# Optimization experiments

Measured on AMD Instinct MI355X. Metric: run time of the kernel, lower is better.

## Reference

```python
import jax, jax.numpy as jnp
import numpy as np

INPUT_SIZE = 128
HIDDEN_SIZE = 1024
OUTPUT_SIZE = 64
E_PROP = 0.8
E_SIZE = int(E_PROP * HIDDEN_SIZE)  # 819
I_SIZE = HIDDEN_SIZE - E_SIZE       # 205


def _make_mask():
    # rows of [+1]*E_SIZE + [-1]*I_SIZE, zero diagonal (no self-connection)
    row = np.concatenate([np.ones(E_SIZE), -np.ones(I_SIZE)]).astype(np.float32)
    mask = np.tile(row, (HIDDEN_SIZE, 1))
    np.fill_diagonal(mask, 0.0)
    return jnp.asarray(mask)


def setup_inputs() -> dict:
    key = jax.random.key(0)
    ks = jax.random.split(key, 8)
    T, B = 512, 64
    scale = 1.0 / np.sqrt(HIDDEN_SIZE)
    x = jax.random.normal(ks[0], (T, B, INPUT_SIZE), dtype=jnp.float32)
    w_ih = jax.random.normal(ks[1], (HIDDEN_SIZE, INPUT_SIZE), dtype=jnp.float32) / np.sqrt(INPUT_SIZE)
    b_ih = jax.random.uniform(ks[2], (HIDDEN_SIZE,), minval=-scale, maxval=scale, dtype=jnp.float32)
    w_hh = jax.random.normal(ks[3], (HIDDEN_SIZE, HIDDEN_SIZE), dtype=jnp.float32) * scale
    # mimic reset_parameters: shrink excitatory columns by e_size/i_size ratio
    w_hh = w_hh.at[:, :E_SIZE].divide(E_SIZE / I_SIZE)
    b_hh = jax.random.uniform(ks[4], (HIDDEN_SIZE,), minval=-scale, maxval=scale, dtype=jnp.float32)
    w_fc = jax.random.normal(ks[5], (OUTPUT_SIZE, E_SIZE), dtype=jnp.float32) / np.sqrt(E_SIZE)
    b_fc = jax.random.uniform(ks[6], (OUTPUT_SIZE,), minval=-scale, maxval=scale, dtype=jnp.float32)
    # NOTE: RNN.__init__ hard-codes alpha = 1 regardless of the value passed in.
    alpha = jnp.array([1.0], dtype=jnp.float32)
    mask = _make_mask()
    return {"x": x, "w_ih": w_ih, "b_ih": b_ih, "w_hh": w_hh, "b_hh": b_hh,
            "w_fc": w_fc, "b_fc": b_fc, "alpha": alpha, "mask": mask}


def reference(x, w_ih, b_ih, w_hh, b_hh, w_fc, b_fc, alpha, mask):
    # x: (T, B, I). Precompute input projection for all timesteps (one big GEMM).
    inp_proj = jnp.einsum('tbi,hi->tbh', x, w_ih) + b_ih  # (T, B, H)
    # effective E-I weight: sign-constrained, zero diagonal; constant across steps
    eff_w = jnp.abs(w_hh) * mask                           # (H, H)
    a = alpha[0]
    B = x.shape[1]
    state0 = jnp.zeros((B, HIDDEN_SIZE), dtype=x.dtype)
    out0 = jnp.zeros((B, HIDDEN_SIZE), dtype=x.dtype)

    def step(carry, u_t):
        state, output = carry
        total = u_t + output @ eff_w.T + b_hh             # (B, H)
        state = a * (total - state) + state               # alpha blend (sigma_rec = 0)
        output = jnp.tanh(state)
        return (state, output), output

    _, rnn_activity = jax.lax.scan(step, (state0, out0), inp_proj)  # (T, B, H)
    rnn_e = rnn_activity[:, :, :E_SIZE]                   # excitatory readout only
    out = jnp.einsum('tbe,oe->tbo', rnn_e, w_fc) + b_fc   # (T, B, O)
    return out, rnn_activity
```

## Files before the change

### kernel.cpp

```cpp
#include <hip/hip_runtime.h>
#include <cmath>

#define T_STEPS 512
#define BATCH   64
#define HID     1024
#define INSZ    128
#define ESZ     819
#define OSZ     64

#define WS_EFFW   0
#define WS_WIHT   1048576
#define WS_HIST   1179648
#define WS_FLAGS  34734080
#define WS_WFCP   34742272

__global__ void prep_effw(const float* __restrict__ w_hh, const float* __restrict__ mask,
                          float* __restrict__ eff) {
    const int i = (blockIdx.x * 256 + threadIdx.x) * 4;
    const float4 w = *(const float4*)(w_hh + i);
    const float4 m = *(const float4*)(mask + i);
    float4 r;
    r.x = fabsf(w.x) * m.x; r.y = fabsf(w.y) * m.y;
    r.z = fabsf(w.z) * m.z; r.w = fabsf(w.w) * m.w;
    *(float4*)(eff + i) = r;
}

__global__ void prep_wihT(const float* __restrict__ w_ih, float* __restrict__ w_ihT) {
    const int idx = blockIdx.x * 256 + threadIdx.x;
    const int i = idx >> 10, h = idx & 1023;
    w_ihT[idx] = w_ih[h * INSZ + i];
}

__global__ void prep_wfc(const float* __restrict__ w_fc, float* __restrict__ w_fcp) {
    const int o = blockIdx.x;
    for (int e = threadIdx.x; e < 820; e += 256)
        w_fcp[o * 820 + e] = (e < ESZ) ? w_fc[o * ESZ + e] : 0.f;
}

__global__ void inp_proj(const float* __restrict__ x, const float* __restrict__ w_ihT,
                         const float* __restrict__ b_ih, float* __restrict__ u) {
    __shared__ float xs[INSZ * 64];
    const int t = blockIdx.x, tid = threadIdx.x;
    const float* xt = x + (size_t)t * BATCH * INSZ;
    for (int k = tid * 4; k < BATCH * INSZ; k += 1024) {
        const float4 v = *(const float4*)(xt + k);
        const int b = k >> 7, i = k & 127;
        xs[(i + 0) * 64 + b] = v.x; xs[(i + 1) * 64 + b] = v.y;
        xs[(i + 2) * 64 + b] = v.z; xs[(i + 3) * 64 + b] = v.w;
    }
    __syncthreads();
    for (int hp = 0; hp < 2; ++hp) {
        const int h = hp * 512 + tid * 2;
        const float bi0 = b_ih[h], bi1 = b_ih[h + 1];
        for (int b0 = 0; b0 < 64; b0 += 8) {
            float acc0[8], acc1[8];
#pragma unroll
            for (int bb = 0; bb < 8; ++bb) { acc0[bb] = 0.f; acc1[bb] = 0.f; }
#pragma unroll 4
            for (int i = 0; i < INSZ; ++i) {
                const float2 w2 = *(const float2*)(w_ihT + i * 1024 + h);
                const float4 xa = *(const float4*)(xs + i * 64 + b0);
                const float4 xb = *(const float4*)(xs + i * 64 + b0 + 4);
                const float xv[8] = {xa.x, xa.y, xa.z, xa.w, xb.x, xb.y, xb.z, xb.w};
#pragma unroll
                for (int bb = 0; bb < 8; ++bb) {
                    acc0[bb] = fmaf(w2.x, xv[bb], acc0[bb]);
                    acc1[bb] = fmaf(w2.y, xv[bb], acc1[bb]);
                }
            }
#pragma unroll
            for (int bb = 0; bb < 8; ++bb) {
                float2 r; r.x = acc0[bb] + bi0; r.y = acc1[bb] + bi1;
                *(float2*)(u + ((size_t)(b0 + bb) * T_STEPS + t) * 1024 + h) = r;
            }
        }
    }
}

__global__ void __launch_bounds__(256, 1)
rnn_scan(const float* __restrict__ eff_w, const float* __restrict__ u,
         const float* __restrict__ b_hh, const float* __restrict__ alpha,
         float* __restrict__ hist, unsigned* __restrict__ flags) {
    extern __shared__ float smem[];
    float* w_s = smem;
    float* pp  = smem + 32768;
    const int tid = threadIdx.x, wg = blockIdx.x;
    const int bg = wg & 7, hgrp = wg >> 3;
    const int h0 = hgrp << 5, b0 = bg << 3;

    {
        const int hl = tid >> 3, grp = hl >> 2, l4 = hl & 3;
        const int j0 = (tid & 7) << 7;
        const float* wrow = eff_w + (size_t)(h0 + hl) * 1024;
        for (int j = j0; j < j0 + 128; j += 4) {
            const float4 w4 = *(const float4*)(wrow + j);
            w_s[((j + 0) << 5) + (((grp + j + 0) & 7) << 2) + l4] = w4.x;
            w_s[((j + 1) << 5) + (((grp + j + 1) & 7) << 2) + l4] = w4.y;
            w_s[((j + 2) << 5) + (((grp + j + 2) & 7) << 2) + l4] = w4.z;
            w_s[((j + 3) << 5) + (((grp + j + 3) & 7) << 2) + l4] = w4.w;
        }
    }
    const float a = alpha[0];
    const int r_hl = tid >> 3, r_b = tid & 7;
    const int rh = h0 + r_hl, rb = b0 + r_b;
    const float bias = b_hh[rh];
    const size_t u_base = ((size_t)rb * T_STEPS) * 1024 + rh;
    float* const my_hist = hist + ((size_t)rb * T_STEPS) * 1024 + rh;
    const int hp = tid >> 5, jc = tid & 31;
    const int sb = tid >> 5, sj = (tid & 31) << 5;
    float state = 0.f;
    __syncthreads();

    for (int t = 0; t < T_STEPS; ++t) {
        const float uval = u[u_base + ((size_t)t << 10)];
        float red = 0.f;
        if (t > 0) {
            {
                const float* src = hist + ((size_t)(b0 + sb) * T_STEPS + (t - 1)) * 1024 + sj;
                float* dst = pp + (sb << 10) + sj;
#pragma unroll
                for (int k = 0; k < 32; k += 4)
                    *(float4*)(dst + k) = *(const float4*)(src + k);
            }
            __syncthreads();
            float acc[4][8];
#pragma unroll
            for (int i = 0; i < 4; ++i)
#pragma unroll
                for (int b = 0; b < 8; ++b) acc[i][b] = 0.f;
#pragma unroll 2
            for (int jj = 0; jj < 32; ++jj) {
                const int j = (jj << 5) + jc;
                const float4 wv = *(const float4*)&w_s[(j << 5) + (((hp + j) & 7) << 2)];
                float pv[8];
#pragma unroll
                for (int b = 0; b < 8; ++b) pv[b] = pp[(b << 10) + j];
#pragma unroll
                for (int b = 0; b < 8; ++b) {
                    acc[0][b] = fmaf(wv.x, pv[b], acc[0][b]);
                    acc[1][b] = fmaf(wv.y, pv[b], acc[1][b]);
                    acc[2][b] = fmaf(wv.z, pv[b], acc[2][b]);
                    acc[3][b] = fmaf(wv.w, pv[b], acc[3][b]);
                }
            }
            __syncthreads();
#pragma unroll
            for (int i = 0; i < 4; ++i)
#pragma unroll
                for (int b = 0; b < 8; ++b) {
                    const int oo = ((hp << 2) + i) * 8 + b;
                    pp[(oo << 5) + ((jc + oo) & 31)] = acc[i][b];
                }
            __syncthreads();
#pragma unroll
            for (int k = 0; k < 32; ++k)
                red += pp[(tid << 5) + ((k + tid) & 31)];
        }
        const float tot = uval + bias + red;
        state = fmaf(a, tot - state, state);
        const float ov = tanhf(state);
        __hip_atomic_store(my_hist + ((size_t)t << 10), ov, __ATOMIC_RELAXED,
                           __HIP_MEMORY_SCOPE_AGENT);
        asm volatile("s_waitcnt vmcnt(0)" ::: "memory");
        __syncthreads();
        if (tid == 0)
            __hip_atomic_store(flags + (wg << 5), (unsigned)(t + 1), __ATOMIC_RELAXED,
                               __HIP_MEMORY_SCOPE_AGENT);
        if (tid < 64) {
            const unsigned tgt = (unsigned)(t + 1);
            for (;;) {
                unsigned v = tgt;
                if (tid < 32)
                    v = __hip_atomic_load(flags + ((bg + (tid << 3)) << 5), __ATOMIC_RELAXED,
                                          __HIP_MEMORY_SCOPE_AGENT);
                if (__ballot(v >= tgt) == ~0ull) break;
                __builtin_amdgcn_s_sleep(4);
            }
        }
        __syncthreads();
    }
}

__global__ void copy_act(const float* __restrict__ hist, float* __restrict__ act) {
    const int t = blockIdx.x >> 6, b = blockIdx.x & 63;
    const float* src = hist + ((size_t)b * T_STEPS + t) * 1024 + threadIdx.x * 4;
    float* dst = act + ((size_t)t * BATCH + b) * 1024 + threadIdx.x * 4;
    *(float4*)dst = *(const float4*)src;
}

__global__ void fc_out(const float* __restrict__ hist, const float* __restrict__ w_fcp,
                       const float* __restrict__ b_fc, float* __restrict__ out0) {
    __shared__ float hs[16 * 820];
    const int t = blockIdx.x >> 2, bq = blockIdx.x & 3, tid = threadIdx.x;
    const int b0 = bq << 4;
    for (int r = 0; r < 16; ++r) {
        const float* src = hist + ((size_t)(b0 + r) * T_STEPS + t) * 1024;
        for (int e = tid; e < 820; e += 256) hs[r * 820 + e] = (e < ESZ) ? src[e] : 0.f;
    }
    __syncthreads();
    const int bb = tid >> 4, ol = tid & 15;
    float acc[4] = {0.f, 0.f, 0.f, 0.f};
    const float* hrow = hs + bb * 820;
    for (int e = 0; e < 820; e += 4) {
        const float4 hv = *(const float4*)(hrow + e);
#pragma unroll
        for (int k = 0; k < 4; ++k) {
            const float4 wv = *(const float4*)(w_fcp + (size_t)(ol + (k << 4)) * 820 + e);
            acc[k] += hv.x * wv.x + hv.y * wv.y + hv.z * wv.z + hv.w * wv.w;
        }
    }
    const int b = b0 + bb;
#pragma unroll
    for (int k = 0; k < 4; ++k) {
        const int o = ol + (k << 4);
        out0[((size_t)t * BATCH + b) * OSZ + o] = acc[k] + b_fc[o];
    }
}

extern "C" void kernel_launch(void* const* d_in, const int* in_sizes, int n_in,
                              void* d_out, int out_size, void* d_ws, size_t ws_size,
                              hipStream_t stream) {
    const float* x     = (const float*)d_in[0];
    const float* w_ih  = (const float*)d_in[1];
    const float* b_ih  = (const float*)d_in[2];
    const float* w_hh  = (const float*)d_in[3];
    const float* b_hh  = (const float*)d_in[4];
    const float* w_fc  = (const float*)d_in[5];
    const float* b_fc  = (const float*)d_in[6];
    const float* alpha = (const float*)d_in[7];
    const float* mask  = (const float*)d_in[8];

    float* out  = (float*)d_out;
    float* out0 = out;
    float* act  = out + (size_t)T_STEPS * BATCH * OSZ;

    float* ws     = (float*)d_ws;
    float* eff_w  = ws + WS_EFFW;
    float* w_ihT  = ws + WS_WIHT;
    float* hist   = ws + WS_HIST;
    unsigned* flags = (unsigned*)(ws + WS_FLAGS);
    float* w_fcp  = ws + WS_WFCP;
    float* u      = act;

    hipMemsetAsync(flags, 0, 8192 * sizeof(unsigned), stream);
    prep_effw<<<1024, 256, 0, stream>>>(w_hh, mask, eff_w);
    prep_wihT<<<512, 256, 0, stream>>>(w_ih, w_ihT);
    prep_wfc<<<64, 256, 0, stream>>>(w_fc, w_fcp);
    inp_proj<<<512, 256, 0, stream>>>(x, w_ihT, b_ih, u);

    hipFuncSetAttribute(reinterpret_cast<const void*>(rnn_scan),
                        hipFuncAttributeMaxDynamicSharedMemorySize, 163840);
    void* args[] = {(void*)&eff_w, (void*)&u, (void*)&b_hh, (void*)&alpha,
                    (void*)&hist, (void*)&flags};
    hipLaunchCooperativeKernel(reinterpret_cast<const void*>(rnn_scan),
                               dim3(256), dim3(256), args, 163840, stream);

    copy_act<<<32768, 256, 0, stream>>>(hist, act);
    fc_out<<<2048, 256, 0, stream>>>(hist, w_fcp, b_fc, out0);
}
```

Baseline: 4.452 ms.

## Replace flag barrier with data-embedded readiness via offset-encoded hidden outputs

Removes the per-step flag-based grid barrier. Each output is stored with a +2 offset, so any value of at least 1 marks it as ready, and consumers spin on the data itself. The offset is folded back out algebraically through adjusted biases in the recurrence (row sums of eff_w) and in the readout (row sums of w_fc), and subtracted in copy_act. This needs a full memset of the history buffer and adds rounding error from the offset, and it also adds an LDS swizzle for the pp staging buffer.

```diff
diff --git a/kernel.cpp b/kernel.cpp
--- a/kernel.cpp
+++ b/kernel.cpp
@@ -11,8 +11,10 @@
 #define WS_EFFW   0
 #define WS_WIHT   1048576
 #define WS_HIST   1179648
-#define WS_FLAGS  34734080
+#define WS_BADJ   34734080
 #define WS_WFCP   34742272
+
+typedef float f32x4 __attribute__((ext_vector_type(4)));
 
 __global__ void prep_effw(const float* __restrict__ w_hh, const float* __restrict__ mask,
                           float* __restrict__ eff) {
@@ -31,10 +33,23 @@
     w_ihT[idx] = w_ih[h * INSZ + i];
 }
 
-__global__ void prep_wfc(const float* __restrict__ w_fc, float* __restrict__ w_fcp) {
-    const int o = blockIdx.x;
-    for (int e = threadIdx.x; e < 820; e += 256)
-        w_fcp[o * 820 + e] = (e < ESZ) ? w_fc[o * ESZ + e] : 0.f;
+__global__ void prep_wfc(const float* __restrict__ w_fc, const float* __restrict__ b_fc,
+                         float* __restrict__ w_fcp, float* __restrict__ badj) {
+    __shared__ float red[256];
+    const int o = blockIdx.x, tid = threadIdx.x;
+    float s = 0.f;
+    for (int e = tid; e < 820; e += 256) {
+        const float w = (e < ESZ) ? w_fc[o * ESZ + e] : 0.f;
+        w_fcp[o * 820 + e] = w;
+        s += w;
+    }
+    red[tid] = s;
+    __syncthreads();
+    for (int st = 128; st; st >>= 1) {
+        if (tid < st) red[tid] += red[tid + st];
+        __syncthreads();
+    }
+    if (tid == 0) badj[o] = b_fc[o] - 2.0f * red[0];
 }
 
 __global__ void inp_proj(const float* __restrict__ x, const float* __restrict__ w_ihT,
@@ -77,10 +92,32 @@
     }
 }
 
+#define LOAD8(SFX)                                                       \
+    asm volatile("global_load_dwordx4 %0, %8, off" SFX "\n\t"            \
+                 "global_load_dwordx4 %1, %8, off offset:16" SFX "\n\t"  \
+                 "global_load_dwordx4 %2, %8, off offset:32" SFX "\n\t"  \
+                 "global_load_dwordx4 %3, %8, off offset:48" SFX "\n\t"  \
+                 "global_load_dwordx4 %4, %8, off offset:64" SFX "\n\t"  \
+                 "global_load_dwordx4 %5, %8, off offset:80" SFX "\n\t"  \
+                 "global_load_dwordx4 %6, %8, off offset:96" SFX "\n\t"  \
+                 "global_load_dwordx4 %7, %8, off offset:112" SFX "\n\t" \
+                 "s_waitcnt vmcnt(0)"                                    \
+                 : "=&v"(v0), "=&v"(v1), "=&v"(v2), "=&v"(v3),           \
+                   "=&v"(v4), "=&v"(v5), "=&v"(v6), "=&v"(v7)            \
+                 : "v"(src) : "memory")
+
+__device__ __forceinline__ float vmin4f(f32x4 v) {
+    return fminf(fminf(v[0], v[1]), fminf(v[2], v[3]));
+}
+
+#define MIN32()                                                              \
+    fminf(fminf(fminf(vmin4f(v0), vmin4f(v1)), fminf(vmin4f(v2), vmin4f(v3))), \
+          fminf(fminf(vmin4f(v4), vmin4f(v5)), fminf(vmin4f(v6), vmin4f(v7))))
+
 __global__ void __launch_bounds__(256, 1)
 rnn_scan(const float* __restrict__ eff_w, const float* __restrict__ u,
          const float* __restrict__ b_hh, const float* __restrict__ alpha,
-         float* __restrict__ hist, unsigned* __restrict__ flags) {
+         float* __restrict__ hist) {
     extern __shared__ float smem[];
     float* w_s = smem;
     float* pp  = smem + 32768;
@@ -88,6 +125,7 @@
     const int bg = wg & 7, hgrp = wg >> 3;
     const int h0 = hgrp << 5, b0 = bg << 3;
 
+    float rsum = 0.f;
     {
         const int hl = tid >> 3, grp = hl >> 2, l4 = hl & 3;
         const int j0 = (tid & 7) << 7;
@@ -98,16 +136,24 @@
             w_s[((j + 1) << 5) + (((grp + j + 1) & 7) << 2) + l4] = w4.y;
             w_s[((j + 2) << 5) + (((grp + j + 2) & 7) << 2) + l4] = w4.z;
             w_s[((j + 3) << 5) + (((grp + j + 3) & 7) << 2) + l4] = w4.w;
+            rsum += (w4.x + w4.y) + (w4.z + w4.w);
         }
     }
+    rsum += __shfl_xor(rsum, 1);
+    rsum += __shfl_xor(rsum, 2);
+    rsum += __shfl_xor(rsum, 4);
+
     const float a = alpha[0];
     const int r_hl = tid >> 3, r_b = tid & 7;
     const int rh = h0 + r_hl, rb = b0 + r_b;
-    const float bias = b_hh[rh];
+    const float bias0 = b_hh[rh];
+    const float bias_eff = bias0 - 2.0f * rsum;
     const size_t u_base = ((size_t)rb * T_STEPS) * 1024 + rh;
     float* const my_hist = hist + ((size_t)rb * T_STEPS) * 1024 + rh;
     const int hp = tid >> 5, jc = tid & 31;
     const int sb = tid >> 5, sj = (tid & 31) << 5;
+    const float* const src_base = hist + ((size_t)(b0 + sb) * T_STEPS) * 1024 + sj;
+    const int rot = tid & 7;
     float state = 0.f;
     __syncthreads();
 
@@ -115,14 +161,26 @@
         const float uval = u[u_base + ((size_t)t << 10)];
         float red = 0.f;
         if (t > 0) {
-            {
-                const float* src = hist + ((size_t)(b0 + sb) * T_STEPS + (t - 1)) * 1024 + sj;
-                float* dst = pp + (sb << 10) + sj;
-#pragma unroll
-                for (int k = 0; k < 32; k += 4)
-                    *(float4*)(dst + k) = *(const float4*)(src + k);
+            f32x4 v0, v1, v2, v3, v4, v5, v6, v7;
+            const float* src = src_base + ((size_t)(t - 1) << 10);
+            LOAD8(" sc0");
+            float mn = MIN32();
+            while (!(mn >= 1.0f)) {
+                __builtin_amdgcn_s_sleep(1);
+                LOAD8(" sc0 sc1");
+                mn = MIN32();
             }
+            float* dst = pp + (sb << 10) + sj;
+            *(f32x4*)(dst + (((rot + 0) & 7) << 2)) = v0;
+            *(f32x4*)(dst + (((rot + 1) & 7) << 2)) = v1;
+            *(f32x4*)(dst + (((rot + 2) & 7) << 2)) = v2;
+            *(f32x4*)(dst + (((rot + 3) & 7) << 2)) = v3;
+            *(f32x4*)(dst + (((rot + 4) & 7) << 2)) = v4;
+            *(f32x4*)(dst + (((rot + 5) & 7) << 2)) = v5;
+            *(f32x4*)(dst + (((rot + 6) & 7) << 2)) = v6;
+            *(f32x4*)(dst + (((rot + 7) & 7) << 2)) = v7;
             __syncthreads();
+
             float acc[4][8];
 #pragma unroll
             for (int i = 0; i < 4; ++i)
@@ -131,16 +189,17 @@
 #pragma unroll 2
             for (int jj = 0; jj < 32; ++jj) {
                 const int j = (jj << 5) + jc;
-                const float4 wv = *(const float4*)&w_s[(j << 5) + (((hp + j) & 7) << 2)];
+                const f32x4 wv = *(const f32x4*)&w_s[(j << 5) + (((hp + j) & 7) << 2)];
+                const int phij = (jj << 5) + ((((jj * 9) + (jc >> 2)) & 7) << 2) + (jc & 3);
                 float pv[8];
 #pragma unroll
-                for (int b = 0; b < 8; ++b) pv[b] = pp[(b << 10) + j];
+                for (int b = 0; b < 8; ++b) pv[b] = pp[(b << 10) + phij];
 #pragma unroll
                 for (int b = 0; b < 8; ++b) {
-                    acc[0][b] = fmaf(wv.x, pv[b], acc[0][b]);
-                    acc[1][b] = fmaf(wv.y, pv[b], acc[1][b]);
-                    acc[2][b] = fmaf(wv.z, pv[b], acc[2][b]);
-                    acc[3][b] = fmaf(wv.w, pv[b], acc[3][b]);
+                    acc[0][b] = fmaf(wv[0], pv[b], acc[0][b]);
+                    acc[1][b] = fmaf(wv[1], pv[b], acc[1][b]);
+                    acc[2][b] = fmaf(wv[2], pv[b], acc[2][b]);
+                    acc[3][b] = fmaf(wv[3], pv[b], acc[3][b]);
                 }
             }
             __syncthreads();
@@ -156,27 +215,11 @@
             for (int k = 0; k < 32; ++k)
                 red += pp[(tid << 5) + ((k + tid) & 31)];
         }
-        const float tot = uval + bias + red;
+        const float tot = uval + red + ((t > 0) ? bias_eff : bias0);
         state = fmaf(a, tot - state, state);
         const float ov = tanhf(state);
-        __hip_atomic_store(my_hist + ((size_t)t << 10), ov, __ATOMIC_RELAXED,
+        __hip_atomic_store(my_hist + ((size_t)t << 10), ov + 2.0f, __ATOMIC_RELAXED,
                            __HIP_MEMORY_SCOPE_AGENT);
-        asm volatile("s_waitcnt vmcnt(0)" ::: "memory");
-        __syncthreads();
-        if (tid == 0)
-            __hip_atomic_store(flags + (wg << 5), (unsigned)(t + 1), __ATOMIC_RELAXED,
-                               __HIP_MEMORY_SCOPE_AGENT);
-        if (tid < 64) {
-            const unsigned tgt = (unsigned)(t + 1);
-            for (;;) {
-                unsigned v = tgt;
-                if (tid < 32)
-                    v = __hip_atomic_load(flags + ((bg + (tid << 3)) << 5), __ATOMIC_RELAXED,
-                                          __HIP_MEMORY_SCOPE_AGENT);
-                if (__ballot(v >= tgt) == ~0ull) break;
-                __builtin_amdgcn_s_sleep(4);
-            }
-        }
         __syncthreads();
     }
 }
@@ -185,11 +228,13 @@
     const int t = blockIdx.x >> 6, b = blockIdx.x & 63;
     const float* src = hist + ((size_t)b * T_STEPS + t) * 1024 + threadIdx.x * 4;
     float* dst = act + ((size_t)t * BATCH + b) * 1024 + threadIdx.x * 4;
-    *(float4*)dst = *(const float4*)src;
+    float4 v = *(const float4*)src;
+    v.x -= 2.0f; v.y -= 2.0f; v.z -= 2.0f; v.w -= 2.0f;
+    *(float4*)dst = v;
 }
 
 __global__ void fc_out(const float* __restrict__ hist, const float* __restrict__ w_fcp,
-                       const float* __restrict__ b_fc, float* __restrict__ out0) {
+                       const float* __restrict__ badj, float* __restrict__ out0) {
     __shared__ float hs[16 * 820];
     const int t = blockIdx.x >> 2, bq = blockIdx.x & 3, tid = threadIdx.x;
     const int b0 = bq << 4;
@@ -213,7 +258,7 @@
 #pragma unroll
     for (int k = 0; k < 4; ++k) {
         const int o = ol + (k << 4);
-        out0[((size_t)t * BATCH + b) * OSZ + o] = acc[k] + b_fc[o];
+        out0[((size_t)t * BATCH + b) * OSZ + o] = acc[k] + badj[o];
     }
 }
 
@@ -238,23 +283,22 @@
     float* eff_w  = ws + WS_EFFW;
     float* w_ihT  = ws + WS_WIHT;
     float* hist   = ws + WS_HIST;
-    unsigned* flags = (unsigned*)(ws + WS_FLAGS);
+    float* badj   = ws + WS_BADJ;
     float* w_fcp  = ws + WS_WFCP;
     float* u      = act;
 
-    hipMemsetAsync(flags, 0, 8192 * sizeof(unsigned), stream);
+    hipMemsetAsync(hist, 0, (size_t)BATCH * T_STEPS * HID * sizeof(float), stream);
     prep_effw<<<1024, 256, 0, stream>>>(w_hh, mask, eff_w);
     prep_wihT<<<512, 256, 0, stream>>>(w_ih, w_ihT);
-    prep_wfc<<<64, 256, 0, stream>>>(w_fc, w_fcp);
+    prep_wfc<<<64, 256, 0, stream>>>(w_fc, b_fc, w_fcp, badj);
     inp_proj<<<512, 256, 0, stream>>>(x, w_ihT, b_ih, u);
 
     hipFuncSetAttribute(reinterpret_cast<const void*>(rnn_scan),
                         hipFuncAttributeMaxDynamicSharedMemorySize, 163840);
-    void* args[] = {(void*)&eff_w, (void*)&u, (void*)&b_hh, (void*)&alpha,
-                    (void*)&hist, (void*)&flags};
+    void* args[] = {(void*)&eff_w, (void*)&u, (void*)&b_hh, (void*)&alpha, (void*)&hist};
     hipLaunchCooperativeKernel(reinterpret_cast<const void*>(rnn_scan),
                                dim3(256), dim3(256), args, 163840, stream);
 
     copy_act<<<32768, 256, 0, stream>>>(hist, act);
-    fc_out<<<2048, 256, 0, stream>>>(hist, w_fcp, b_fc, out0);
-}
+    fc_out<<<2048, 256, 0, stream>>>(hist, w_fcp, badj, out0);
+}
```

New measurement: 4.953 ms. +11.3%, slower.
